# Kernel optimization log

Hardware: AMD Instinct MI355X
Metric: run time of the kernel (lower is better)

## Reference

```python
import jax, jax.numpy as jnp
import numpy as np

COST_CLASS = 2.0
COST_SCREW_MID = 5.0
COST_SCREW_HEAD_TIP = 5.0
GAMMA = 2.0
EPS = 1e-8


def _l1_cdist(a, b):
    # a: [N, d], b: [T, d] -> [N, T] pairwise L1 distance
    return jnp.abs(a[:, None, :] - b[None, :, :]).sum(-1)


def _midpoint(s):
    # screw parameterized as (head_xy, tip_xy); midpoint of the segment
    return (s[:, :2] + s[:, 2:]) * 0.5


def setup_inputs() -> dict:
    key = jax.random.key(0)
    k1, k2, k3, k4 = jax.random.split(key, 4)
    bs, nq, nc = 32, 900, 2
    tpi = 30  # targets per image
    total_tgt = bs * tpi
    return {
        "pred_logits": jax.random.normal(k1, (bs, nq, nc), dtype=jnp.float32),
        "pred_screws": jax.random.uniform(k2, (bs, nq, 4), dtype=jnp.float32),
        "tgt_labels": jax.random.randint(k3, (total_tgt,), 0, nc),
        "tgt_screws": jax.random.uniform(k4, (total_tgt, 4), dtype=jnp.float32),
        "num_targets_per_image": tpi,
    }


def reference(pred_logits, pred_screws, tgt_labels, tgt_screws, num_targets_per_image):
    bs, nq, nc = pred_logits.shape
    out_prob = jax.nn.sigmoid(pred_logits.reshape(bs * nq, nc))  # [N, C]
    out_screws = pred_screws.reshape(bs * nq, 4)                 # [N, 4]

    # focal-style classification cost, gathered at target class ids
    neg_cost = out_prob ** GAMMA * -jnp.log1p(-(out_prob - EPS))  # -log(1 - p + eps)
    pos_cost = (1.0 - out_prob) ** GAMMA * -jnp.log(out_prob + EPS)
    cost_class = pos_cost[:, tgt_labels] - neg_cost[:, tgt_labels]  # [N, T]

    # geometric costs: L1 on midpoint, plus L1 on head and tip endpoints
    cost_mid = _l1_cdist(_midpoint(out_screws), _midpoint(tgt_screws))
    cost_head_tip = (_l1_cdist(out_screws[:, :2], tgt_screws[:, :2])
                     + _l1_cdist(out_screws[:, 2:], tgt_screws[:, 2:]))

    C = (COST_SCREW_MID * cost_mid
         + COST_CLASS * cost_class
         + COST_SCREW_HEAD_TIP * cost_head_tip)
    return C.reshape(bs, nq, -1)  # [bs, num_queries, total_targets]
```

## Files before the change

kernel.cpp:

```cpp
#include <hip/hip_runtime.h>
#include <math.h>


#define NB 16
#define BLOCK 256

__global__ __launch_bounds__(BLOCK) void matcher_kernel(
    const float* __restrict__ logits,
    const float* __restrict__ pscrews,
    const int*   __restrict__ tlabels,
    const float* __restrict__ tscrews,
    float*       __restrict__ out,
    int N, int T)
{
    __shared__ float row[NB][8];
    const int tid = threadIdx.x;
    const int n0  = blockIdx.x * NB;

    if (tid < NB && (n0 + tid) < N) {
        const int n = n0 + tid;
        float4 s = reinterpret_cast<const float4*>(pscrews)[n];
        float hx = s.x, hy = s.y, tx = s.z, ty = s.w;
        row[tid][0] = hx; row[tid][1] = hy;
        row[tid][2] = tx; row[tid][3] = ty;
        row[tid][4] = (hx + tx) * 0.5f;
        row[tid][5] = (hy + ty) * 0.5f;
        float l0 = logits[n * 2 + 0];
        float l1 = logits[n * 2 + 1];
        #pragma unroll
        for (int c = 0; c < 2; ++c) {
            float l = (c == 0) ? l0 : l1;
            float p = 1.0f / (1.0f + expf(-l));
            float om = 1.0f - p;
            float pos = om * om * (-logf(p + 1e-8f));
            float neg = p * p * (-logf(1.0f - p + 1e-8f));
            row[tid][6 + c] = 2.0f * (pos - neg);
        }
    }

    const int chunk = tid;
    const bool active = (chunk * 4 + 3) < T;
    float thx[4], thy[4], ttx[4], tty[4], tmx[4], tmy[4];
    int   lab[4];
    if (active) {
        int4 lb = reinterpret_cast<const int4*>(tlabels)[chunk];
        lab[0] = lb.x; lab[1] = lb.y; lab[2] = lb.z; lab[3] = lb.w;
        #pragma unroll
        for (int j = 0; j < 4; ++j) {
            float4 s = reinterpret_cast<const float4*>(tscrews)[chunk * 4 + j];
            thx[j] = s.x; thy[j] = s.y; ttx[j] = s.z; tty[j] = s.w;
            tmx[j] = (s.x + s.z) * 0.5f;
            tmy[j] = (s.y + s.w) * 0.5f;
        }
    }

    __syncthreads();

    if (!active) return;

    for (int r = 0; r < NB; ++r) {
        const int n = n0 + r;
        if (n >= N) break;
        float4 a = *reinterpret_cast<const float4*>(&row[r][0]);
        float4 b = *reinterpret_cast<const float4*>(&row[r][4]);
        float4 res;
        float v[4];
        #pragma unroll
        for (int j = 0; j < 4; ++j) {
            float d = fabsf(a.x - thx[j]) + fabsf(a.y - thy[j])
                    + fabsf(a.z - ttx[j]) + fabsf(a.w - tty[j])
                    + fabsf(b.x - tmx[j]) + fabsf(b.y - tmy[j]);
            float cc = (lab[j] != 0) ? b.w : b.z;
            v[j] = fmaf(d, 5.0f, cc);
        }
        res.x = v[0]; res.y = v[1]; res.z = v[2]; res.w = v[3];
        reinterpret_cast<float4*>(out)[(n * T) / 4 + chunk] = res;
    }
}

extern "C" void kernel_launch(void* const* d_in, const int* in_sizes, int n_in,
                              void* d_out, int out_size, void* d_ws, size_t ws_size,
                              hipStream_t stream) {
    const float* logits  = (const float*)d_in[0];
    const float* pscrews = (const float*)d_in[1];
    const int*   tlabels = (const int*)d_in[2];
    const float* tscrews = (const float*)d_in[3];
    float* out = (float*)d_out;

    const int N = in_sizes[1] / 4;
    const int T = in_sizes[2];

    const int blocks = (N + NB - 1) / NB;
    matcher_kernel<<<blocks, BLOCK, 0, stream>>>(logits, pscrews, tlabels, tscrews, out, N, T);
}
```

Measured before the change: 124.7 us.

## Split into row-descriptor precompute and flat grid-stride streaming store kernel

Replaces the per-block shared-memory row staging with two kernels. The first precomputes per-query descriptors (endpoints, midpoint, class costs) into workspace. The second is a flat streaming kernel where each thread writes one float4 output chunk, with row and chunk found by a magic-number division and the store marked nontemporal. The aim is full occupancy and fully coalesced output writes without a __syncthreads barrier, at the cost of an extra launch and reloading target data per thread, with a fused fallback when no workspace is available.

```diff
diff --git a/kernel.cpp b/kernel.cpp
--- a/kernel.cpp
+++ b/kernel.cpp
@@ -1,81 +1,105 @@
 #include <hip/hip_runtime.h>
 #include <math.h>
+#include <stdint.h>
 
 
-#define NB 16
 #define BLOCK 256
 
-__global__ __launch_bounds__(BLOCK) void matcher_kernel(
+typedef float f32x4 __attribute__((ext_vector_type(4)));
+
+__device__ __forceinline__ float class_cost(float l) {
+    float p  = 1.0f / (1.0f + expf(-l));
+    float om = 1.0f - p;
+    float pos = om * om * (-logf(p + 1e-8f));
+    float neg = p * p * (-logf(om + 1e-8f));
+    return 2.0f * (pos - neg);
+}
+
+__global__ __launch_bounds__(BLOCK) void row_desc_kernel(
+    const float* __restrict__ logits,
+    const float* __restrict__ pscrews,
+    float*       __restrict__ ws,
+    int N)
+{
+    int n = blockIdx.x * BLOCK + threadIdx.x;
+    if (n >= N) return;
+    float4 s = reinterpret_cast<const float4*>(pscrews)[n];
+    float2 l = reinterpret_cast<const float2*>(logits)[n];
+    f32x4 d0 = {s.x, s.y, s.z, s.w};
+    f32x4 d1 = {(s.x + s.z) * 0.5f, (s.y + s.w) * 0.5f, class_cost(l.x), class_cost(l.y)};
+    f32x4* w = reinterpret_cast<f32x4*>(ws) + (size_t)n * 2;
+    w[0] = d0;
+    w[1] = d1;
+}
+
+__global__ __launch_bounds__(BLOCK) void stream_kernel(
+    const float* __restrict__ ws,
+    const int*   __restrict__ tlabels,
+    const float* __restrict__ tscrews,
+    float*       __restrict__ out,
+    unsigned total, unsigned TQ, unsigned long long M)
+{
+    unsigned g = blockIdx.x * BLOCK + threadIdx.x;
+    if (g >= total) return;
+    unsigned row   = (unsigned)(((unsigned long long)g * M) >> 38);
+    unsigned chunk = g - row * TQ;
+
+    f32x4 a = reinterpret_cast<const f32x4*>(ws)[(size_t)row * 2 + 0];
+    f32x4 b = reinterpret_cast<const f32x4*>(ws)[(size_t)row * 2 + 1];
+    int4 lb = reinterpret_cast<const int4*>(tlabels)[chunk];
+    int labs[4] = {lb.x, lb.y, lb.z, lb.w};
+
+    float v[4];
+    #pragma unroll
+    for (int j = 0; j < 4; ++j) {
+        float4 s = reinterpret_cast<const float4*>(tscrews)[(size_t)chunk * 4 + j];
+        float tmx = (s.x + s.z) * 0.5f;
+        float tmy = (s.y + s.w) * 0.5f;
+        float d = fabsf(a.x - s.x) + fabsf(a.y - s.y)
+                + fabsf(a.z - s.z) + fabsf(a.w - s.w)
+                + fabsf(b.x - tmx) + fabsf(b.y - tmy);
+        float cc = (labs[j] != 0) ? b.w : b.z;
+        v[j] = fmaf(d, 5.0f, cc);
+    }
+    f32x4 res = {v[0], v[1], v[2], v[3]};
+    __builtin_nontemporal_store(res, reinterpret_cast<f32x4*>(out) + g);
+}
+
+__global__ __launch_bounds__(BLOCK) void fused_kernel(
     const float* __restrict__ logits,
     const float* __restrict__ pscrews,
     const int*   __restrict__ tlabels,
     const float* __restrict__ tscrews,
     float*       __restrict__ out,
-    int N, int T)
+    unsigned total, unsigned TQ, unsigned long long M)
 {
-    __shared__ float row[NB][8];
-    const int tid = threadIdx.x;
-    const int n0  = blockIdx.x * NB;
+    unsigned g = blockIdx.x * BLOCK + threadIdx.x;
+    if (g >= total) return;
+    unsigned row   = (unsigned)(((unsigned long long)g * M) >> 38);
+    unsigned chunk = g - row * TQ;
 
-    if (tid < NB && (n0 + tid) < N) {
-        const int n = n0 + tid;
-        float4 s = reinterpret_cast<const float4*>(pscrews)[n];
-        float hx = s.x, hy = s.y, tx = s.z, ty = s.w;
-        row[tid][0] = hx; row[tid][1] = hy;
-        row[tid][2] = tx; row[tid][3] = ty;
-        row[tid][4] = (hx + tx) * 0.5f;
-        row[tid][5] = (hy + ty) * 0.5f;
-        float l0 = logits[n * 2 + 0];
-        float l1 = logits[n * 2 + 1];
-        #pragma unroll
-        for (int c = 0; c < 2; ++c) {
-            float l = (c == 0) ? l0 : l1;
-            float p = 1.0f / (1.0f + expf(-l));
-            float om = 1.0f - p;
-            float pos = om * om * (-logf(p + 1e-8f));
-            float neg = p * p * (-logf(1.0f - p + 1e-8f));
-            row[tid][6 + c] = 2.0f * (pos - neg);
-        }
+    float4 s0 = reinterpret_cast<const float4*>(pscrews)[row];
+    float2 l  = reinterpret_cast<const float2*>(logits)[row];
+    float mx = (s0.x + s0.z) * 0.5f, my = (s0.y + s0.w) * 0.5f;
+    float cc0 = class_cost(l.x), cc1 = class_cost(l.y);
+
+    int4 lb = reinterpret_cast<const int4*>(tlabels)[chunk];
+    int labs[4] = {lb.x, lb.y, lb.z, lb.w};
+
+    float v[4];
+    #pragma unroll
+    for (int j = 0; j < 4; ++j) {
+        float4 s = reinterpret_cast<const float4*>(tscrews)[(size_t)chunk * 4 + j];
+        float tmx = (s.x + s.z) * 0.5f;
+        float tmy = (s.y + s.w) * 0.5f;
+        float d = fabsf(s0.x - s.x) + fabsf(s0.y - s.y)
+                + fabsf(s0.z - s.z) + fabsf(s0.w - s.w)
+                + fabsf(mx - tmx) + fabsf(my - tmy);
+        float cc = (labs[j] != 0) ? cc1 : cc0;
+        v[j] = fmaf(d, 5.0f, cc);
     }
-
-    const int chunk = tid;
-    const bool active = (chunk * 4 + 3) < T;
-    float thx[4], thy[4], ttx[4], tty[4], tmx[4], tmy[4];
-    int   lab[4];
-    if (active) {
-        int4 lb = reinterpret_cast<const int4*>(tlabels)[chunk];
-        lab[0] = lb.x; lab[1] = lb.y; lab[2] = lb.z; lab[3] = lb.w;
-        #pragma unroll
-        for (int j = 0; j < 4; ++j) {
-            float4 s = reinterpret_cast<const float4*>(tscrews)[chunk * 4 + j];
-            thx[j] = s.x; thy[j] = s.y; ttx[j] = s.z; tty[j] = s.w;
-            tmx[j] = (s.x + s.z) * 0.5f;
-            tmy[j] = (s.y + s.w) * 0.5f;
-        }
-    }
-
-    __syncthreads();
-
-    if (!active) return;
-
-    for (int r = 0; r < NB; ++r) {
-        const int n = n0 + r;
-        if (n >= N) break;
-        float4 a = *reinterpret_cast<const float4*>(&row[r][0]);
-        float4 b = *reinterpret_cast<const float4*>(&row[r][4]);
-        float4 res;
-        float v[4];
-        #pragma unroll
-        for (int j = 0; j < 4; ++j) {
-            float d = fabsf(a.x - thx[j]) + fabsf(a.y - thy[j])
-                    + fabsf(a.z - ttx[j]) + fabsf(a.w - tty[j])
-                    + fabsf(b.x - tmx[j]) + fabsf(b.y - tmy[j]);
-            float cc = (lab[j] != 0) ? b.w : b.z;
-            v[j] = fmaf(d, 5.0f, cc);
-        }
-        res.x = v[0]; res.y = v[1]; res.z = v[2]; res.w = v[3];
-        reinterpret_cast<float4*>(out)[(n * T) / 4 + chunk] = res;
-    }
+    f32x4 res = {v[0], v[1], v[2], v[3]};
+    __builtin_nontemporal_store(res, reinterpret_cast<f32x4*>(out) + g);
 }
 
 extern "C" void kernel_launch(void* const* d_in, const int* in_sizes, int n_in,
@@ -89,7 +113,19 @@
 
     const int N = in_sizes[1] / 4;
     const int T = in_sizes[2];
+    const unsigned TQ = (unsigned)(T / 4);
+    const unsigned total = (unsigned)N * TQ;
+    const unsigned long long M = ((1ULL << 38) + TQ - 1) / TQ;
 
-    const int blocks = (N + NB - 1) / NB;
-    matcher_kernel<<<blocks, BLOCK, 0, stream>>>(logits, pscrews, tlabels, tscrews, out, N, T);
+    const int blocksB = (int)((total + BLOCK - 1) / BLOCK);
+
+    if (ws_size >= (size_t)N * 8 * sizeof(float)) {
+        const int blocksA = (N + BLOCK - 1) / BLOCK;
+        row_desc_kernel<<<blocksA, BLOCK, 0, stream>>>(logits, pscrews, (float*)d_ws, N);
+        stream_kernel<<<blocksB, BLOCK, 0, stream>>>((const float*)d_ws, tlabels, tscrews,
+                                                     out, total, TQ, M);
+    } else {
+        fused_kernel<<<blocksB, BLOCK, 0, stream>>>(logits, pscrews, tlabels, tscrews,
+                                                    out, total, TQ, M);
+    }
 }
```

Result: slower. 149.0 us (+19.5%).
